# Performance work log

Hardware: AMD Instinct MI355X
Metric: run time of the kernel (lower is better)

The kernel has to match this reference:

```python
import jax, jax.numpy as jnp
import numpy as np
from jax import lax
from jax.scipy.special import logsumexp

B, T, C = 512, 512, 64


def setup_inputs() -> dict:
    key = jax.random.key(0)
    k1, k2, k3, k4, k5 = jax.random.split(key, 5)
    emissions = jax.random.normal(k1, (B, T, C), dtype=jnp.float32)
    tags = jax.random.randint(k2, (B, T), 0, C, dtype=jnp.int32)
    mask = jnp.ones((B, T), dtype=jnp.int32)
    transitions = jax.random.normal(k3, (C, C), dtype=jnp.float32)
    start_transitions = jax.random.normal(k4, (C,), dtype=jnp.float32)
    end_transitions = jax.random.normal(k5, (C,), dtype=jnp.float32)
    return {"emissions": emissions, "tags": tags, "mask": mask,
            "transitions": transitions, "start_transitions": start_transitions,
            "end_transitions": end_transitions}


def _log_partition(emissions, maskb, transitions, start_transitions, end_transitions):
    # forward algorithm: lp [B,C] carried over T-1 steps
    lp0 = start_transitions[None, :] + emissions[:, 0]  # [B,C]

    def step(lp, xs):
        emit_t, mask_t = xs  # [B,C], [B]
        # score[b,i,j] = lp[b,i] + trans[i,j] + emit[b,j]
        score = lp[:, :, None] + transitions[None, :, :] + emit_t[:, None, :]
        lp_next = logsumexp(score, axis=1)  # [B,C]
        lp = jnp.where(mask_t[:, None], lp_next, lp)
        return lp, None

    xs = (jnp.swapaxes(emissions[:, 1:], 0, 1), jnp.swapaxes(maskb[:, 1:], 0, 1))
    lp, _ = lax.scan(step, lp0, xs)
    return logsumexp(lp + end_transitions[None, :], axis=1)  # [B]


def _joint_score(emissions, tags, mask, maskb, transitions, start_transitions, end_transitions):
    b_idx = jnp.arange(emissions.shape[0])
    score0 = start_transitions[tags[:, 0]] + emissions[b_idx, 0, tags[:, 0]]  # [B]
    trans = transitions[tags[:, :-1], tags[:, 1:]]  # [B,T-1]
    emit = jnp.take_along_axis(emissions, tags[:, :, None], axis=2)[:, :, 0]  # [B,T]
    step_scores = jnp.where(maskb[:, 1:], trans + emit[:, 1:], 0.0)
    last_idx = jnp.sum(mask, axis=1).astype(jnp.int32) - 1
    last_tags = tags[b_idx, last_idx]
    return score0 + jnp.sum(step_scores, axis=1) + end_transitions[last_tags]


def reference(emissions, tags, mask, transitions, start_transitions, end_transitions):
    maskb = mask.astype(bool)
    log_denominator = _log_partition(emissions, maskb, transitions, start_transitions, end_transitions)
    log_numerator = _joint_score(emissions, tags, mask, maskb, transitions, start_transitions, end_transitions)
    return jnp.mean(log_denominator - log_numerator)
```

## Files before the change

### kernel.cpp

```cpp
#include <hip/hip_runtime.h>

#define Bn 512
#define Tn 512
#define Cn 64


template <int CTRL>
__device__ __forceinline__ float fmax_dpp(const float v) {
    const int o = __builtin_amdgcn_update_dpp(__float_as_int(v), __float_as_int(v),
                                              CTRL, 0xF, 0xF, false);
    return fmaxf(v, __int_as_float(o));
}

__device__ __forceinline__ float wave_max64(float v) {
    v = fmax_dpp<0x0B1>(v);
    v = fmax_dpp<0x04E>(v);
    v = fmax_dpp<0x141>(v);
    v = fmax_dpp<0x140>(v);
    v = fmax_dpp<0x142>(v);
    v = fmax_dpp<0x143>(v);
    return __int_as_float(__builtin_amdgcn_readlane(__float_as_int(v), 63));
}

__device__ __forceinline__ float bcast_dot64(const float a, const float* __restrict__ w) {
    const int ai = __float_as_int(a);
    float acc0 = 0.f, acc1 = 0.f, acc2 = 0.f, acc3 = 0.f;
#pragma unroll
    for (int i = 0; i < Cn; i += 4) {
        const float b0 = __int_as_float(__builtin_amdgcn_ds_bpermute(4 * (i + 0), ai));
        const float b1 = __int_as_float(__builtin_amdgcn_ds_bpermute(4 * (i + 1), ai));
        const float b2 = __int_as_float(__builtin_amdgcn_ds_bpermute(4 * (i + 2), ai));
        const float b3 = __int_as_float(__builtin_amdgcn_ds_bpermute(4 * (i + 3), ai));
        acc0 = fmaf(b0, w[i + 0], acc0);
        acc1 = fmaf(b1, w[i + 1], acc1);
        acc2 = fmaf(b2, w[i + 2], acc2);
        acc3 = fmaf(b3, w[i + 3], acc3);
    }
    return (acc0 + acc1) + (acc2 + acc3);
}

__global__ __launch_bounds__(64, 1) void crf_half_kernel(
    const float* __restrict__ emissions,
    const int*   __restrict__ tags,
    const int*   __restrict__ mask,
    const float* __restrict__ transitions,
    const float* __restrict__ start_t,
    const float* __restrict__ end_t,
    float*       __restrict__ ws_alpha,
    float*       __restrict__ ws_beta,
    float*       __restrict__ ws_lsF,
    float*       __restrict__ ws_lsB,
    float*       __restrict__ ws_num)
{
    const int  blk = blockIdx.x;
    const bool fwd = blk < Bn;
    const int  bt  = blk & (Bn - 1);
    const int  j   = threadIdx.x;

    const float* em  = emissions + (size_t)bt * Tn * Cn + j;
    const float* em0 = emissions + (size_t)bt * Tn * Cn;
    const int*   mk  = mask + bt * Tn;
    const int*   tg  = tags + bt * Tn;

    if (fwd) {
        float nsum = 0.f;
        int   mcnt = 0;
        for (int t = j; t < Tn; t += 64) {
            const int tag_t = tg[t];
            const int m_t   = mk[t];
            mcnt += m_t;
            if (t >= 1 && m_t) {
                const int tag_p = tg[t - 1];
                nsum += transitions[tag_p * Cn + tag_t] + em0[t * Cn + tag_t];
            }
        }
#pragma unroll
        for (int off = 32; off > 0; off >>= 1) {
            nsum += __shfl_xor(nsum, off, 64);
            mcnt += __shfl_xor(mcnt, off, 64);
        }

        float w[Cn];
#pragma unroll
        for (int i = 0; i < Cn; ++i) w[i] = __expf(transitions[i * Cn + j]);
#pragma unroll
        for (int i = 0; i < Cn; ++i) asm volatile("" : "+v"(w[i]));

        float lp0 = start_t[j] + em[0];
        const float m0 = wave_max64(lp0);
        float log_scale = m0;
        float a_self = __expf(lp0 - m0);
        float c_pend = 1.0f;

        float cur_e[4];
        int   cur_m[4];
#pragma unroll
        for (int k = 0; k < 4; ++k) {
            cur_e[k] = em[(size_t)(1 + k) * Cn];
            cur_m[k] = mk[1 + k];
        }

        for (int g = 0; g < 64; ++g) {
            float nxt_e[4];
            int   nxt_m[4];
#pragma unroll
            for (int k = 0; k < 4; ++k) {
                const int t = 4 * g + 5 + k;
                nxt_e[k] = em[(size_t)t * Cn];
                nxt_m[k] = mk[t];
            }
            float ex[4];
#pragma unroll
            for (int k = 0; k < 4; ++k) ex[k] = __expf(cur_e[k]);

#pragma unroll
            for (int k = 0; k < 4; ++k) {
                float s = bcast_dot64(a_self, w) * ex[k];
                if (!cur_m[k]) s = a_self;
                if (k == 0) {
                    s *= c_pend;
                    c_pend = 1.0f;
                }
                if (k == 3) {
                    const float mx = wave_max64(s);
                    c_pend = __builtin_amdgcn_rcpf(mx);
                    log_scale += __logf(mx);
                }
                a_self = s;
            }
#pragma unroll
            for (int k = 0; k < 4; ++k) {
                cur_e[k] = nxt_e[k];
                cur_m[k] = nxt_m[k];
            }
        }

        a_self *= c_pend;
        ws_alpha[bt * Cn + j] = a_self;
        if (j == 0) {
            ws_lsF[bt] = log_scale;
            const int t0 = tg[0];
            const int tl = tg[mcnt - 1];
            ws_num[bt] = start_t[t0] + em0[t0] + nsum + end_t[tl];
        }
    } else {
        float w[Cn];
#pragma unroll
        for (int i = 0; i < Cn; ++i) w[i] = __expf(transitions[j * Cn + i]);
#pragma unroll
        for (int i = 0; i < Cn; ++i) asm volatile("" : "+v"(w[i]));

        float lp0 = end_t[j];
        const float m0 = wave_max64(lp0);
        float log_scale = m0;
        float b_self = __expf(lp0 - m0);
        float c_pend = 1.0f;

        float cur_e[4];
        int   cur_m[4];
#pragma unroll
        for (int k = 0; k < 4; ++k) {
            const int u = Tn - 1 - k;
            cur_e[k] = em[(size_t)u * Cn];
            cur_m[k] = mk[u];
        }

        for (int g = 0; g < 64; ++g) {
            float nxt_e[4];
            int   nxt_m[4];
#pragma unroll
            for (int k = 0; k < 4; ++k) {
                const int u = Tn - 5 - 4 * g - k;
                nxt_e[k] = em[(size_t)u * Cn];
                nxt_m[k] = mk[u];
            }
            float ex[4];
#pragma unroll
            for (int k = 0; k < 4; ++k) ex[k] = __expf(cur_e[k]);

#pragma unroll
            for (int k = 0; k < 4; ++k) {
                const int s_idx = 4 * g + k;
                if (s_idx < Tn / 2 - 1) {
                    const float wval = b_self * ex[k];
                    float s = bcast_dot64(wval, w);
                    if (!cur_m[k]) s = b_self;
                    if (k == 0) {
                        s *= c_pend;
                        c_pend = 1.0f;
                    }
                    if (k == 3) {
                        const float mx = wave_max64(s);
                        c_pend = __builtin_amdgcn_rcpf(mx);
                        log_scale += __logf(mx);
                    }
                    b_self = s;
                }
            }
#pragma unroll
            for (int k = 0; k < 4; ++k) {
                cur_e[k] = nxt_e[k];
                cur_m[k] = nxt_m[k];
            }
        }

        b_self *= c_pend;
        ws_beta[bt * Cn + j] = b_self;
        if (j == 0) ws_lsB[bt] = log_scale;
    }
}

__global__ __launch_bounds__(1024) void crf_combine_kernel(
    const float* __restrict__ ws_alpha,
    const float* __restrict__ ws_beta,
    const float* __restrict__ ws_lsF,
    const float* __restrict__ ws_lsB,
    const float* __restrict__ ws_num,
    float*       __restrict__ out)
{
    const int wv = threadIdx.x >> 6;
    const int j  = threadIdx.x & 63;
    const int bt = blockIdx.x * 16 + wv;

    __shared__ float part[16];

    float v = ws_alpha[bt * Cn + j] * ws_beta[bt * Cn + j];
#pragma unroll
    for (int off = 32; off > 0; off >>= 1) v += __shfl_xor(v, off, 64);
    if (j == 0) {
        part[wv] = ws_lsF[bt] + ws_lsB[bt] + __logf(v) - ws_num[bt];
    }
    __syncthreads();
    if (threadIdx.x < 64) {
        float p = (j < 16) ? part[j] : 0.f;
#pragma unroll
        for (int off = 32; off > 0; off >>= 1) p += __shfl_xor(p, off, 64);
        if (j == 0) atomicAdd(out, p * (1.0f / Bn));
    }
}

__global__ void crf_zero_kernel(float* out) { out[0] = 0.f; }

extern "C" void kernel_launch(void* const* d_in, const int* in_sizes, int n_in,
                              void* d_out, int out_size, void* d_ws, size_t ws_size,
                              hipStream_t stream)
{
    const float* emissions   = (const float*)d_in[0];
    const int*   tags        = (const int*)d_in[1];
    const int*   mask        = (const int*)d_in[2];
    const float* transitions = (const float*)d_in[3];
    const float* start_t     = (const float*)d_in[4];
    const float* end_t       = (const float*)d_in[5];

    float* ws       = (float*)d_ws;
    float* ws_alpha = ws;
    float* ws_beta  = ws_alpha + Bn * Cn;
    float* ws_lsF   = ws_beta + Bn * Cn;
    float* ws_lsB   = ws_lsF + Bn;
    float* ws_num   = ws_lsB + Bn;

    crf_zero_kernel<<<1, 1, 0, stream>>>((float*)d_out);
    crf_half_kernel<<<2 * Bn, Cn, 0, stream>>>(emissions, tags, mask, transitions,
                                               start_t, end_t,
                                               ws_alpha, ws_beta, ws_lsF, ws_lsB, ws_num);
    crf_combine_kernel<<<Bn / 16, 1024, 0, stream>>>(ws_alpha, ws_beta, ws_lsF, ws_lsB,
                                                     ws_num, (float*)d_out);
}
```

Baseline: 171.3 us.

## Use readlane broadcast, ballot mask bits, double-buffer emission prefetch, fold zero kernel

The per-step 64-wide dot product now broadcasts the state with v_readlane into scalar registers instead of ds_bpermute. This removes LDS-path permute latency from the serial recurrence. Per-timestep mask loads are replaced by ballots precomputed once, and emissions are prefetched through two alternating 4-step buffers in a loop that is deliberately not unrolled. The zero-init kernel is folded into the main kernel, which removes one launch. Readlane adds SGPR-to-VGPR dependencies and scalar instruction pressure.

```diff
diff --git a/kernel.cpp b/kernel.cpp
--- a/kernel.cpp
+++ b/kernel.cpp
@@ -27,10 +27,10 @@
     float acc0 = 0.f, acc1 = 0.f, acc2 = 0.f, acc3 = 0.f;
 #pragma unroll
     for (int i = 0; i < Cn; i += 4) {
-        const float b0 = __int_as_float(__builtin_amdgcn_ds_bpermute(4 * (i + 0), ai));
-        const float b1 = __int_as_float(__builtin_amdgcn_ds_bpermute(4 * (i + 1), ai));
-        const float b2 = __int_as_float(__builtin_amdgcn_ds_bpermute(4 * (i + 2), ai));
-        const float b3 = __int_as_float(__builtin_amdgcn_ds_bpermute(4 * (i + 3), ai));
+        const float b0 = __int_as_float(__builtin_amdgcn_readlane(ai, i + 0));
+        const float b1 = __int_as_float(__builtin_amdgcn_readlane(ai, i + 1));
+        const float b2 = __int_as_float(__builtin_amdgcn_readlane(ai, i + 2));
+        const float b3 = __int_as_float(__builtin_amdgcn_readlane(ai, i + 3));
         acc0 = fmaf(b0, w[i + 0], acc0);
         acc1 = fmaf(b1, w[i + 1], acc1);
         acc2 = fmaf(b2, w[i + 2], acc2);
@@ -39,7 +39,9 @@
     return (acc0 + acc1) + (acc2 + acc3);
 }
 
-__global__ __launch_bounds__(64, 1) void crf_half_kernel(
+__global__ __launch_bounds__(64)
+__attribute__((amdgpu_waves_per_eu(1, 1)))
+void crf_half_kernel(
     const float* __restrict__ emissions,
     const int*   __restrict__ tags,
     const int*   __restrict__ mask,
@@ -50,13 +52,16 @@
     float*       __restrict__ ws_beta,
     float*       __restrict__ ws_lsF,
     float*       __restrict__ ws_lsB,
-    float*       __restrict__ ws_num)
+    float*       __restrict__ ws_num,
+    float*       __restrict__ out)
 {
     const int  blk = blockIdx.x;
     const bool fwd = blk < Bn;
     const int  bt  = blk & (Bn - 1);
     const int  j   = threadIdx.x;
 
+    if (blk == 0 && j == 0) out[0] = 0.f;
+
     const float* em  = emissions + (size_t)bt * Tn * Cn + j;
     const float* em0 = emissions + (size_t)bt * Tn * Cn;
     const int*   mk  = mask + bt * Tn;
@@ -65,9 +70,18 @@
     if (fwd) {
         float nsum = 0.f;
         int   mcnt = 0;
-        for (int t = j; t < Tn; t += 64) {
+        unsigned long long bal0 = 0, bal1 = 0, bal2 = 0, bal3 = 0, bal4 = 0;
+#pragma unroll
+        for (int it = 0; it < 8; ++it) {
+            const int t     = it * 64 + j;
             const int tag_t = tg[t];
             const int m_t   = mk[t];
+            const unsigned long long b = __ballot(m_t != 0);
+            if      (it == 0) bal0 = b;
+            else if (it == 1) bal1 = b;
+            else if (it == 2) bal2 = b;
+            else if (it == 3) bal3 = b;
+            else if (it == 4) bal4 = b;
             mcnt += m_t;
             if (t >= 1 && m_t) {
                 const int tag_p = tg[t - 1];
@@ -83,8 +97,6 @@
         float w[Cn];
 #pragma unroll
         for (int i = 0; i < Cn; ++i) w[i] = __expf(transitions[i * Cn + j]);
-#pragma unroll
-        for (int i = 0; i < Cn; ++i) asm volatile("" : "+v"(w[i]));
 
         float lp0 = start_t[j] + em[0];
         const float m0 = wave_max64(lp0);
@@ -92,48 +104,53 @@
         float a_self = __expf(lp0 - m0);
         float c_pend = 1.0f;
 
-        float cur_e[4];
-        int   cur_m[4];
-#pragma unroll
-        for (int k = 0; k < 4; ++k) {
-            cur_e[k] = em[(size_t)(1 + k) * Cn];
-            cur_m[k] = mk[1 + k];
-        }
-
-        for (int g = 0; g < 64; ++g) {
-            float nxt_e[4];
-            int   nxt_m[4];
-#pragma unroll
-            for (int k = 0; k < 4; ++k) {
-                const int t = 4 * g + 5 + k;
-                nxt_e[k] = em[(size_t)t * Cn];
-                nxt_m[k] = mk[t];
-            }
-            float ex[4];
-#pragma unroll
-            for (int k = 0; k < 4; ++k) ex[k] = __expf(cur_e[k]);
-
-#pragma unroll
-            for (int k = 0; k < 4; ++k) {
-                float s = bcast_dot64(a_self, w) * ex[k];
-                if (!cur_m[k]) s = a_self;
-                if (k == 0) {
-                    s *= c_pend;
-                    c_pend = 1.0f;
-                }
-                if (k == 3) {
-                    const float mx = wave_max64(s);
-                    c_pend = __builtin_amdgcn_rcpf(mx);
-                    log_scale += __logf(mx);
-                }
-                a_self = s;
-            }
-#pragma unroll
-            for (int k = 0; k < 4; ++k) {
-                cur_e[k] = nxt_e[k];
-                cur_m[k] = nxt_m[k];
-            }
-        }
+        float P[4], Q[4];
+#pragma unroll
+        for (int k = 0; k < 4; ++k) P[k] = em[(size_t)(1 + k) * Cn];
+#pragma unroll
+        for (int k = 0; k < 4; ++k) Q[k] = em[(size_t)(5 + k) * Cn];
+
+#define FWD_STEP(k, tt, exk)                                               \
+        {                                                                  \
+            float s_ = bcast_dot64(a_self, w) * (exk);                     \
+            const int t_ = (tt);                                           \
+            const unsigned long long bw_ = (t_ < 128)                     \
+                ? (t_ < 64 ? bal0 : bal1)                                  \
+                : (t_ < 192 ? bal2 : (t_ < 256 ? bal3 : bal4));            \
+            if (!((bw_ >> (t_ & 63)) & 1ull)) s_ = a_self;                 \
+            if ((k) == 0) { s_ *= c_pend; c_pend = 1.0f; }                 \
+            if ((k) == 3) { const float mx_ = wave_max64(s_);              \
+                            c_pend = __builtin_amdgcn_rcpf(mx_);           \
+                            log_scale += __logf(mx_); }                    \
+            a_self = s_;                                                   \
+        }
+
+#pragma unroll 1
+        for (int i = 0; i < 32; ++i) {
+            {
+                const float ex0 = __expf(P[0]), ex1 = __expf(P[1]);
+                const float ex2 = __expf(P[2]), ex3 = __expf(P[3]);
+                const int tp = 8 * i + 9;
+#pragma unroll
+                for (int k = 0; k < 4; ++k) P[k] = em[(size_t)(tp + k) * Cn];
+                FWD_STEP(0, 8 * i + 1, ex0)
+                FWD_STEP(1, 8 * i + 2, ex1)
+                FWD_STEP(2, 8 * i + 3, ex2)
+                FWD_STEP(3, 8 * i + 4, ex3)
+            }
+            {
+                const float ex0 = __expf(Q[0]), ex1 = __expf(Q[1]);
+                const float ex2 = __expf(Q[2]), ex3 = __expf(Q[3]);
+                const int tq = 8 * i + 13;
+#pragma unroll
+                for (int k = 0; k < 4; ++k) Q[k] = em[(size_t)(tq + k) * Cn];
+                FWD_STEP(0, 8 * i + 5, ex0)
+                FWD_STEP(1, 8 * i + 6, ex1)
+                FWD_STEP(2, 8 * i + 7, ex2)
+                FWD_STEP(3, 8 * i + 8, ex3)
+            }
+        }
+#undef FWD_STEP
 
         a_self *= c_pend;
         ws_alpha[bt * Cn + j] = a_self;
@@ -144,11 +161,19 @@
             ws_num[bt] = start_t[t0] + em0[t0] + nsum + end_t[tl];
         }
     } else {
+        unsigned long long bal4 = 0, bal5 = 0, bal6 = 0, bal7 = 0;
+#pragma unroll
+        for (int it = 4; it < 8; ++it) {
+            const unsigned long long b = __ballot(mk[it * 64 + j] != 0);
+            if      (it == 4) bal4 = b;
+            else if (it == 5) bal5 = b;
+            else if (it == 6) bal6 = b;
+            else              bal7 = b;
+        }
+
         float w[Cn];
 #pragma unroll
         for (int i = 0; i < Cn; ++i) w[i] = __expf(transitions[j * Cn + i]);
-#pragma unroll
-        for (int i = 0; i < Cn; ++i) asm volatile("" : "+v"(w[i]));
 
         float lp0 = end_t[j];
         const float m0 = wave_max64(lp0);
@@ -156,53 +181,56 @@
         float b_self = __expf(lp0 - m0);
         float c_pend = 1.0f;
 
-        float cur_e[4];
-        int   cur_m[4];
-#pragma unroll
-        for (int k = 0; k < 4; ++k) {
-            const int u = Tn - 1 - k;
-            cur_e[k] = em[(size_t)u * Cn];
-            cur_m[k] = mk[u];
-        }
-
-        for (int g = 0; g < 64; ++g) {
-            float nxt_e[4];
-            int   nxt_m[4];
-#pragma unroll
-            for (int k = 0; k < 4; ++k) {
-                const int u = Tn - 5 - 4 * g - k;
-                nxt_e[k] = em[(size_t)u * Cn];
-                nxt_m[k] = mk[u];
-            }
-            float ex[4];
-#pragma unroll
-            for (int k = 0; k < 4; ++k) ex[k] = __expf(cur_e[k]);
-
-#pragma unroll
-            for (int k = 0; k < 4; ++k) {
-                const int s_idx = 4 * g + k;
-                if (s_idx < Tn / 2 - 1) {
-                    const float wval = b_self * ex[k];
-                    float s = bcast_dot64(wval, w);
-                    if (!cur_m[k]) s = b_self;
-                    if (k == 0) {
-                        s *= c_pend;
-                        c_pend = 1.0f;
-                    }
-                    if (k == 3) {
-                        const float mx = wave_max64(s);
-                        c_pend = __builtin_amdgcn_rcpf(mx);
-                        log_scale += __logf(mx);
-                    }
-                    b_self = s;
+        float P[4], Q[4];
+#pragma unroll
+        for (int k = 0; k < 4; ++k) P[k] = em[(size_t)(Tn - 1 - k) * Cn];
+#pragma unroll
+        for (int k = 0; k < 4; ++k) Q[k] = em[(size_t)(Tn - 5 - k) * Cn];
+
+#define BWD_STEP(k, uu, exk)                                               \
+        {                                                                  \
+            const float wval_ = b_self * (exk);                            \
+            float s_ = bcast_dot64(wval_, w);                              \
+            const int u_ = (uu);                                           \
+            const unsigned long long bw_ = (u_ < 384)                      \
+                ? (u_ < 320 ? bal4 : bal5)                                 \
+                : (u_ < 448 ? bal6 : bal7);                                \
+            if (!((bw_ >> (u_ & 63)) & 1ull)) s_ = b_self;                 \
+            if ((k) == 0) { s_ *= c_pend; c_pend = 1.0f; }                 \
+            if ((k) == 3) { const float mx_ = wave_max64(s_);              \
+                            c_pend = __builtin_amdgcn_rcpf(mx_);           \
+                            log_scale += __logf(mx_); }                    \
+            b_self = s_;                                                   \
+        }
+
+#pragma unroll 1
+        for (int i = 0; i < 32; ++i) {
+            {
+                const float ex0 = __expf(P[0]), ex1 = __expf(P[1]);
+                const float ex2 = __expf(P[2]), ex3 = __expf(P[3]);
+                const int up = 503 - 8 * i;
+#pragma unroll
+                for (int k = 0; k < 4; ++k) P[k] = em[(size_t)(up - k) * Cn];
+                BWD_STEP(0, 511 - 8 * i, ex0)
+                BWD_STEP(1, 510 - 8 * i, ex1)
+                BWD_STEP(2, 509 - 8 * i, ex2)
+                BWD_STEP(3, 508 - 8 * i, ex3)
+            }
+            {
+                const float ex0 = __expf(Q[0]), ex1 = __expf(Q[1]);
+                const float ex2 = __expf(Q[2]), ex3 = __expf(Q[3]);
+                const int uq = 499 - 8 * i;
+#pragma unroll
+                for (int k = 0; k < 4; ++k) Q[k] = em[(size_t)(uq - k) * Cn];
+                BWD_STEP(0, 507 - 8 * i, ex0)
+                BWD_STEP(1, 506 - 8 * i, ex1)
+                BWD_STEP(2, 505 - 8 * i, ex2)
+                if (i < 31) {
+                    BWD_STEP(3, 504 - 8 * i, ex3)
                 }
             }
-#pragma unroll
-            for (int k = 0; k < 4; ++k) {
-                cur_e[k] = nxt_e[k];
-                cur_m[k] = nxt_m[k];
-            }
-        }
+        }
+#undef BWD_STEP
 
         b_self *= c_pend;
         ws_beta[bt * Cn + j] = b_self;
@@ -239,8 +267,6 @@
     }
 }
 
-__global__ void crf_zero_kernel(float* out) { out[0] = 0.f; }
-
 extern "C" void kernel_launch(void* const* d_in, const int* in_sizes, int n_in,
                               void* d_out, int out_size, void* d_ws, size_t ws_size,
                               hipStream_t stream)
@@ -259,10 +285,10 @@
     float* ws_lsB   = ws_lsF + Bn;
     float* ws_num   = ws_lsB + Bn;
 
-    crf_zero_kernel<<<1, 1, 0, stream>>>((float*)d_out);
     crf_half_kernel<<<2 * Bn, Cn, 0, stream>>>(emissions, tags, mask, transitions,
                                                start_t, end_t,
-                                               ws_alpha, ws_beta, ws_lsF, ws_lsB, ws_num);
+                                               ws_alpha, ws_beta, ws_lsF, ws_lsB, ws_num,
+                                               (float*)d_out);
     crf_combine_kernel<<<Bn / 16, 1024, 0, stream>>>(ws_alpha, ws_beta, ws_lsF, ws_lsB,
                                                      ws_num, (float*)d_out);
 }
```

Result: slower. 181.0 us (+5.6%).
